# Kernel tuning notes

Measured on AMD Instinct MI355X. Metric: run time of the kernel, lower is better.

Reference implementation:

```python
import jax, jax.numpy as jnp
import numpy as np

EPS = 1e-6

def setup_inputs() -> dict:
    key = jax.random.key(0)
    ks = jax.random.split(key, 5)
    B, H, N, D = 4, 8, 8192, 64
    q = jax.random.uniform(ks[0], (B, H, N, D), dtype=jnp.float32)
    k = jax.random.uniform(ks[1], (B, H, N, D), dtype=jnp.float32)
    q_rot = jax.random.uniform(ks[2], (B, H, N, D), dtype=jnp.float32)
    k_rot = jax.random.uniform(ks[3], (B, H, N, D), dtype=jnp.float32)
    v = jax.random.normal(ks[4], (B, H, N, D), dtype=jnp.float32)
    return {"q": q, "k": k, "q_rot": q_rot, "k_rot": k_rot, "v": v, "chunk_size": 128}


def _chunked_causal_linear_attention(q, k, q_rot, k_rot, v, chunk_size):
    # Faithful port of infer_hidden_states: chunked causal linear attention
    # with cumsum kernel trick and recurrent state carry-over.
    B, H, N, D = q.shape
    E = v.shape[-1]
    C = chunk_size
    nc = N // C

    def to_chunks(x):
        # [B,H,N,d] -> [nc,B,H,C,d]
        return jnp.moveaxis(x.reshape(B, H, nc, C, x.shape[-1]), 2, 0)

    qc, kc, qrc, krc, vc = map(to_chunks, (q, k, q_rot, k_rot, v))

    init = (
        jnp.zeros((B, H, 1, D), q.dtype),        # last_k_cumsum
        jnp.zeros((B, H, 1, D, E), q.dtype),     # last_context_cumsum
        jnp.zeros((B, H, 1, D), q.dtype),        # last_k_cumsum_rot
        jnp.zeros((B, H, 1, D, E), q.dtype),     # last_context_cumsum_rot
    )

    def step(carry, inp):
        last_k, last_S, last_k_rot, last_S_rot = carry
        qi, ki, qri, kri, vi = inp                  # [B,H,C,*]
        k_cs = last_k + jnp.cumsum(ki, axis=-2)     # [B,H,C,D]
        k_cs_rot = last_k_rot + jnp.cumsum(kri, axis=-2)
        Dn = jnp.einsum('bhnd,bhnd->bhn', qi, k_cs)
        Dr = jnp.einsum('bhnd,bhnd->bhn', qri, k_cs_rot)
        D_inv = 1.0 / (Dn + Dr + EPS)               # [B,H,C]
        ctx = jnp.einsum('bhnd,bhne->bhnde', ki, vi)
        S = last_S + jnp.cumsum(ctx, axis=2)        # [B,H,C,D,E]
        ctx_rot = jnp.einsum('bhnd,bhne->bhnde', kri, vi)
        S_rot = last_S_rot + jnp.cumsum(ctx_rot, axis=2)
        out = jnp.einsum('bhnde,bhnd,bhn->bhne', S, qi, D_inv)
        out = out + jnp.einsum('bhnde,bhnd,bhn->bhne', S_rot, qri, D_inv)
        new_carry = (k_cs[:, :, -1:], S[:, :, -1:], k_cs_rot[:, :, -1:], S_rot[:, :, -1:])
        return new_carry, out

    (Z, S, Z_rot, S_rot), outs = jax.lax.scan(step, init, (qc, kc, qrc, krc, vc))
    out = jnp.moveaxis(outs, 0, 2).reshape(B, H, N, E)
    # states: squeeze chunk dim as in torch (squeeze(2))
    return out, Z[:, :, 0], S[:, :, 0], Z_rot[:, :, 0], S_rot[:, :, 0]


def reference(q, k, q_rot, k_rot, v, chunk_size):
    return _chunked_causal_linear_attention(q, k, q_rot, k_rot, v, chunk_size)
```

## Files before the change

kernel.cpp:

```cpp
#include <hip/hip_runtime.h>


typedef short bf16x8 __attribute__((ext_vector_type(8)));
typedef float f32x4  __attribute__((ext_vector_type(4)));
union U16x8 { bf16x8 v; uint4 u; };

constexpr int BH = 32;
constexpr int N_ = 8192, D_ = 64, E_ = 64, C_ = 128;
constexpr int NC = 64;
constexpr int NCHUNKS = BH * NC;
constexpr int STATE = 8320;
#define EPS_ 1e-6f

constexpr size_t OUT_ELEMS = (size_t)BH * N_ * E_;
constexpr size_t ZOFF  = OUT_ELEMS;
constexpr size_t SOFF  = ZOFF  + (size_t)BH * 64;
constexpr size_t ZROFF = SOFF  + (size_t)BH * 4096;
constexpr size_t SROFF = ZROFF + (size_t)BH * 64;

__device__ inline unsigned cvt2(float a, float b){
    union { float f; unsigned u; } x, y; x.f = a; y.f = b;
    unsigned lo = (x.u + 0x7fffu + ((x.u >> 16) & 1u)) >> 16;
    unsigned hi = (y.u + 0x7fffu + ((y.u >> 16) & 1u)) >> 16;
    return lo | (hi << 16);
}
__device__ inline unsigned short cvt1(float a){
    union { float f; unsigned u; } x; x.f = a;
    return (unsigned short)((x.u + 0x7fffu + ((x.u >> 16) & 1u)) >> 16);
}
__device__ inline float bflo(float x, unsigned short hi){
    union { unsigned u; float f; } h; h.u = ((unsigned)hi) << 16;
    return x - h.f;
}

constexpr int TILE = 520;
#define MFMA(A,B,C) __builtin_amdgcn_mfma_f32_16x16x32_bf16((A),(B),(C),0,0,0)

constexpr int AKH = 0, AKL = 8, ARH = 16, ARL = 24, BVH = 32, BVL = 40, BON = 48;
constexpr int SM1_TOT = 50 * TILE;

__global__ __launch_bounds__(256, 3) void chunk_states(
    const float* __restrict__ gk, const float* __restrict__ gkr,
    const float* __restrict__ gv, float* __restrict__ ws)
{
    __shared__ unsigned short sm[SM1_TOT];
    const int t = threadIdx.x;
    const int cid = blockIdx.x, bh = cid >> 6, c = cid & 63;
    const size_t gbase = (size_t)bh * N_ * D_ + (size_t)c * C_ * D_;
    const int w = t >> 6, lane = t & 63, lg = lane >> 4, lm = lane & 15;
    const int col = t & 63, r0g = (t >> 6) * 16;

    float kv[16], krv[16], vv[16];
    auto load_half = [&](int h){
        const size_t base = gbase + (size_t)(h * 64 + r0g) * D_ + col;
#pragma unroll
        for (int i = 0; i < 16; ++i) {
            kv [i] = gk [base + (size_t)i * D_];
            krv[i] = gkr[base + (size_t)i * D_];
            vv [i] = gv [base + (size_t)i * D_];
        }
    };
    auto write_hl = [&](const float* v16, int hiT, int loT){
#pragma unroll
        for (int hh = 0; hh < 2; ++hh) {
            const int rr = r0g + 8 * hh;
            const int tile = (rr >> 5) * 4 + (col >> 4);
            const int off = ((col & 15) + 16 * ((rr & 31) >> 3)) * 8;
            unsigned short h8[8]; float l8[8];
#pragma unroll
            for (int j = 0; j < 8; ++j) {
                h8[j] = cvt1(v16[8*hh + j]);
                l8[j] = bflo(v16[8*hh + j], h8[j]);
            }
            uint4 uh = make_uint4((unsigned)h8[0] | ((unsigned)h8[1] << 16),
                                  (unsigned)h8[2] | ((unsigned)h8[3] << 16),
                                  (unsigned)h8[4] | ((unsigned)h8[5] << 16),
                                  (unsigned)h8[6] | ((unsigned)h8[7] << 16));
            uint4 ul = make_uint4(cvt2(l8[0],l8[1]), cvt2(l8[2],l8[3]),
                                  cvt2(l8[4],l8[5]), cvt2(l8[6],l8[7]));
            *(uint4*)&sm[(hiT + tile) * TILE + off] = uh;
            *(uint4*)&sm[(loT + tile) * TILE + off] = ul;
        }
    };

    for (int i = t; i < 2 * TILE; i += 256) {
        const int tile = i / TILE, off = i % TILE;
        unsigned short val = (off < 512 && ((off >> 3) & 15) == 0) ? (unsigned short)0x3F80 : (unsigned short)0;
        sm[(BON + tile) * TILE + off] = val;
    }

    f32x4 aK[4], aR[4], sK = {0.f,0.f,0.f,0.f}, sR = {0.f,0.f,0.f,0.f};
#pragma unroll
    for (int e = 0; e < 4; ++e) { aK[e] = f32x4{0.f,0.f,0.f,0.f}; aR[e] = f32x4{0.f,0.f,0.f,0.f}; }

    auto FR = [&](int tile)->bf16x8 { return *(const bf16x8*)&sm[tile * TILE + lane * 8]; };
    auto compute = [&](){
#pragma unroll
        for (int kt = 0; kt < 2; ++kt) {
            bf16x8 ah = FR(AKH + kt*4 + w), al = FR(AKL + kt*4 + w);
            bf16x8 rh = FR(ARH + kt*4 + w), rl = FR(ARL + kt*4 + w);
            bf16x8 bo = FR(BON + kt);
            sK = MFMA(ah, bo, sK); sK = MFMA(al, bo, sK);
            sR = MFMA(rh, bo, sR); sR = MFMA(rl, bo, sR);
#pragma unroll
            for (int et = 0; et < 4; ++et) {
                bf16x8 bh = FR(BVH + kt*4 + et), bl = FR(BVL + kt*4 + et);
                aK[et] = MFMA(ah, bh, aK[et]);
                aK[et] = MFMA(al, bh, aK[et]);
                aK[et] = MFMA(ah, bl, aK[et]);
                aR[et] = MFMA(rh, bh, aR[et]);
                aR[et] = MFMA(rl, bh, aR[et]);
                aR[et] = MFMA(rh, bl, aR[et]);
            }
        }
    };

    load_half(0);
    write_hl(kv, AKH, AKL); write_hl(krv, ARH, ARL); write_hl(vv, BVH, BVL);
    load_half(1);
    __syncthreads();
    compute();
    __syncthreads();
    write_hl(kv, AKH, AKL); write_hl(krv, ARH, ARL); write_hl(vv, BVH, BVL);
    __syncthreads();
    compute();

    float* st = ws + (size_t)cid * STATE;
    if (lm == 0) {
#pragma unroll
        for (int r = 0; r < 4; ++r) {
            const int d = w*16 + lg*4 + r;
            st[d]      = sK[r];
            st[64 + d] = sR[r];
        }
    }
    float* cs  = st + 128;
    float* csr = st + 128 + 4096;
#pragma unroll
    for (int et = 0; et < 4; ++et)
#pragma unroll
        for (int r = 0; r < 4; ++r) {
            const int d = w*16 + lg*4 + r, e = et*16 + lm;
            cs [d*64 + e] = aK[et][r];
            csr[d*64 + e] = aR[et][r];
        }
}

__global__ __launch_bounds__(256) void scan_states(float* __restrict__ ws, float* __restrict__ out)
{
    const int bh = blockIdx.x;
    const int j4 = blockIdx.y * 256 + threadIdx.x;
    if (j4 >= STATE / 4) return;
    float4 run = make_float4(0.f, 0.f, 0.f, 0.f);
    float* base = ws + (size_t)bh * NC * STATE + (size_t)j4 * 4;
#pragma unroll 8
    for (int c = 0; c < NC; ++c) {
        float4 x = *(float4*)(base + (size_t)c * STATE);
        *(float4*)(base + (size_t)c * STATE) = run;
        run.x += x.x; run.y += x.y; run.z += x.z; run.w += x.w;
    }
    const int j = j4 * 4;
    float* dst;
    if (j < 64)        dst = out + ZOFF  + (size_t)bh*64   + j;
    else if (j < 128)  dst = out + ZROFF + (size_t)bh*64   + (j - 64);
    else if (j < 4224) dst = out + SOFF  + (size_t)bh*4096 + (j - 128);
    else               dst = out + SROFF + (size_t)bh*4096 + (j - 4224);
    *(float4*)dst = run;
}

constexpr int SK0 = 0, SV0 = 16, SP0 = 24, SSC0 = 0;
constexpr int SM3_TOT = 32 * TILE;

#define KFRG(ten,td,tm)  (*(const bf16x8*)&sm[(SK0 + ((ten)*2+(td))*4+(tm))*TILE + lane*8])
#define VFRG(tk,te)      (*(const bf16x8*)&sm[(SV0 + (tk)*4+(te))*TILE + lane*8])
#define SCFRG(ten,td,te) (*(const bf16x8*)&sm[(SSC0 + (ten)*10+(td)*5+(te))*TILE + lane*8])

__device__ inline void stage_colT(const float* src, int ldr, unsigned short* dst, int mr, int mc){
    const int t = threadIdx.x;
    const int col = t & 63, r0 = (t >> 6) * 16;
    float v[16];
#pragma unroll
    for (int i = 0; i < 16; ++i) v[i] = src[(size_t)(r0 + i) * ldr + col];
#pragma unroll
    for (int h = 0; h < 2; ++h) {
        const int rr = r0 + 8 * h;
        const int tile = (rr >> 5) * mr + (col >> 4) * mc;
        uint4 u = make_uint4(cvt2(v[8*h+0],v[8*h+1]), cvt2(v[8*h+2],v[8*h+3]),
                             cvt2(v[8*h+4],v[8*h+5]), cvt2(v[8*h+6],v[8*h+7]));
        *(uint4*)&dst[tile*TILE + ((col&15) + 16*((rr&31)>>3))*8] = u;
    }
}

__global__ __launch_bounds__(256, 4) void chunk_out(
    const float* __restrict__ gq, const float* __restrict__ gqr,
    const float* __restrict__ gk, const float* __restrict__ gkr,
    const float* __restrict__ gv, const float* __restrict__ ws,
    float* __restrict__ out)
{
    __shared__ unsigned short sm[SM3_TOT];
    const int t = threadIdx.x;
    const int blk = blockIdx.x, chunk = blk >> 1, rbk = blk & 1;
    const int bh = chunk >> 6, c = chunk & 63;
    const size_t gbase = (size_t)bh * N_ * D_ + (size_t)c * C_ * D_;
    const float* st = ws + (size_t)chunk * STATE;
    const int w = t >> 6, lane = t & 63, lg = lane >> 4, lm = lane & 15;
    const int col = t & 63, r0g = (t >> 6) * 16;

    bf16x8 qf[2][2];
    {
        const size_t qrow = gbase + (size_t)(rbk*64 + w*16 + lm) * D_;
#pragma unroll
        for (int td = 0; td < 2; ++td) {
            const size_t g = qrow + td*32 + lg*8;
            float4 a = *(const float4*)(gq + g),  b = *(const float4*)(gq + g + 4);
            float4 ar= *(const float4*)(gqr + g), br= *(const float4*)(gqr + g + 4);
            U16x8 u;
            u.u = make_uint4(cvt2(a.x,a.y), cvt2(a.z,a.w), cvt2(b.x,b.y), cvt2(b.z,b.w));
            qf[0][td] = u.v;
            u.u = make_uint4(cvt2(ar.x,ar.y), cvt2(ar.z,ar.w), cvt2(br.x,br.y), cvt2(br.z,br.w));
            qf[1][td] = u.v;
        }
    }

    float4 kf4[4], rf4[4];
    auto load_kr = [&](int mh){
        const size_t g = gbase + (size_t)(mh*64 + (t >> 2)) * D_ + (t & 3)*16;
#pragma unroll
        for (int i = 0; i < 4; ++i) {
            kf4[i] = *(const float4*)(gk  + g + i*4);
            rf4[i] = *(const float4*)(gkr + g + i*4);
        }
    };
    auto write_row_reg = [&](const float4* f, int baseT, int mr, int mc){
        const int r = t >> 2, c0 = (t & 3) * 16;
        const int tile = (r >> 4) * mr + (c0 >> 5) * mc;
        const int g0 = (c0 & 31) >> 3;
        uint4 u0 = make_uint4(cvt2(f[0].x,f[0].y), cvt2(f[0].z,f[0].w),
                              cvt2(f[1].x,f[1].y), cvt2(f[1].z,f[1].w));
        uint4 u1 = make_uint4(cvt2(f[2].x,f[2].y), cvt2(f[2].z,f[2].w),
                              cvt2(f[3].x,f[3].y), cvt2(f[3].z,f[3].w));
        *(uint4*)&sm[(baseT + tile)*TILE + ((r&15) + 16* g0   )*8] = u0;
        *(uint4*)&sm[(baseT + tile)*TILE + ((r&15) + 16*(g0+1))*8] = u1;
    };
    auto stage_v = [&](int mh){
        float vv[16];
        const size_t base = gbase + (size_t)(mh*64 + r0g) * D_ + col;
#pragma unroll
        for (int i = 0; i < 16; ++i) vv[i] = gv[base + (size_t)i * D_];
#pragma unroll
        for (int hh = 0; hh < 2; ++hh) {
            const int rr = r0g + 8*hh;
            const int tile = (rr >> 5) * 4 + (col >> 4);
            uint4 u = make_uint4(cvt2(vv[8*hh+0],vv[8*hh+1]), cvt2(vv[8*hh+2],vv[8*hh+3]),
                                 cvt2(vv[8*hh+4],vv[8*hh+5]), cvt2(vv[8*hh+6],vv[8*hh+7]));
            *(uint4*)&sm[(SV0 + tile)*TILE + ((col&15) + 16*((rr&31)>>3))*8] = u;
        }
    };

    f32x4 oacc[4];
#pragma unroll
    for (int te = 0; te < 4; ++te) oacc[te] = f32x4{0.f,0.f,0.f,0.f};
    f32x4 acc4 = f32x4{0.f,0.f,0.f,0.f};
    float denp[4] = {0.f,0.f,0.f,0.f};

    const int TMmax = rbk * 4 + w;
    const int TKtop = ((TMmax >> 1) << 1) + 1;

    auto compute_half = [&](int mh){
#pragma unroll
        for (int tm = 0; tm < 4; ++tm) {
            const int TM = mh*4 + tm;
            if (TM <= TKtop) {
                f32x4 a = f32x4{0.f,0.f,0.f,0.f};
                if (TM <= TMmax) {
                    a = MFMA(qf[0][0], KFRG(0,0,tm), a);
                    a = MFMA(qf[0][1], KFRG(0,1,tm), a);
                    a = MFMA(qf[1][0], KFRG(1,0,tm), a);
                    a = MFMA(qf[1][1], KFRG(1,1,tm), a);
                }
                const int mb = TM * 16 + lm;
                const int pb = (SP0 + w*2 + (tm>>1))*TILE
                             + 16*((tm&1)*2 + (lm>>3))*8 + (lm&7);
#pragma unroll
                for (int r = 0; r < 4; ++r) {
                    const int ng = rbk*64 + w*16 + lg*4 + r;
                    const float pv = (TM <= TMmax && mb <= ng) ? a[r] : 0.f;
                    denp[r] += pv;
                    sm[pb + (lg*4 + r)*8] = cvt1(pv);
                }
            }
        }
#pragma unroll
        for (int tk = 0; tk < 2; ++tk) {
            const int TK = mh*2 + tk;
            if (TK <= (TMmax >> 1)) {
                bf16x8 pa = *(const bf16x8*)&sm[(SP0 + w*2+tk)*TILE + lane*8];
#pragma unroll
                for (int te = 0; te < 4; ++te)
                    oacc[te] = MFMA(pa, VFRG(tk,te), oacc[te]);
            }
        }
    };

    load_kr(0);
    write_row_reg(kf4, SK0, 1, 4);
    write_row_reg(rf4, SK0 + 8, 1, 4);
    stage_v(0);
    if (rbk) load_kr(1);
    __syncthreads();
    compute_half(0);
    if (rbk) {
        __syncthreads();
        write_row_reg(kf4, SK0, 1, 4);
        write_row_reg(rf4, SK0 + 8, 1, 4);
        stage_v(1);
        __syncthreads();
        compute_half(1);
    }

    __syncthreads();
    stage_colT(st + 128,        64, sm + SSC0*TILE,             5, 1);
    stage_colT(st + 128 + 4096, 64, sm + (SSC0 + 10)*TILE,      5, 1);
    for (int i = t; i < 4 * 260; i += 256) {
        const int tile = i / 260, off = i % 260;
        const int ten = tile >> 1, td = tile & 1;
        *(unsigned*)&sm[(SSC0 + ten*10 + td*5 + 4)*TILE + off*2] = 0u;
    }
    __syncthreads();
    if (t < 128) {
        const int ten = t >> 6, d = t & 63;
        sm[(SSC0 + ten*10 + (d>>5)*5 + 4)*TILE + (16*((d&31)>>3))*8 + (d&7)] = cvt1(st[t]);
    }
    __syncthreads();
#pragma unroll
    for (int td = 0; td < 2; ++td) {
#pragma unroll
        for (int te = 0; te < 4; ++te) {
            oacc[te] = MFMA(qf[0][td], SCFRG(0,td,te), oacc[te]);
            oacc[te] = MFMA(qf[1][td], SCFRG(1,td,te), oacc[te]);
        }
        acc4 = MFMA(qf[0][td], SCFRG(0,td,4), acc4);
        acc4 = MFMA(qf[1][td], SCFRG(1,td,4), acc4);
    }

    const size_t orow = (size_t)bh * N_ * E_ + (size_t)(c * C_ + rbk * 64 + w * 16) * E_;
#pragma unroll
    for (int r = 0; r < 4; ++r) {
        float d = denp[r];
        d += __shfl_xor(d, 1); d += __shfl_xor(d, 2);
        d += __shfl_xor(d, 4); d += __shfl_xor(d, 8);
        const float dc = __shfl(acc4[r], lane & 48);
        const float dinv = 1.0f / (d + dc + EPS_);
        const size_t ob = orow + (size_t)(lg * 4 + r) * E_ + lm;
        out[ob +  0] = oacc[0][r] * dinv;
        out[ob + 16] = oacc[1][r] * dinv;
        out[ob + 32] = oacc[2][r] * dinv;
        out[ob + 48] = oacc[3][r] * dinv;
    }
}
#undef KFRG
#undef VFRG
#undef SCFRG

extern "C" void kernel_launch(void* const* d_in, const int* in_sizes, int n_in,
                              void* d_out, int out_size, void* d_ws, size_t ws_size,
                              hipStream_t stream) {
    const float* q  = (const float*)d_in[0];
    const float* k  = (const float*)d_in[1];
    const float* qr = (const float*)d_in[2];
    const float* kr = (const float*)d_in[3];
    const float* v  = (const float*)d_in[4];
    float* out = (float*)d_out;
    float* ws  = (float*)d_ws;

    chunk_states<<<NCHUNKS, 256, 0, stream>>>(k, kr, v, ws);
    scan_states<<<dim3(BH, 9), 256, 0, stream>>>(ws, out);
    chunk_out<<<NCHUNKS * 2, 256, 0, stream>>>(q, qr, k, kr, v, ws, out);
}
```

Measured before the change: 398.4 us.

## Merge chunk_out row halves into one 512-thread block and build constant fragments in registers

chunk_out now runs one 512-thread block per chunk instead of two 256-thread blocks that each restaged K/Kr/V. The shared K/V tiles are loaded once per half, and warps whose rows precede the current half skip its compute. The ones-fragment and the Z-augmentation fragment are now built in registers rather than staged through shared memory. Each state tile is prefetched into registers before the intra-chunk loop. This removes duplicated global loads and several syncs, at the cost of more LDS per block and load imbalance across the eight warps.

```diff
diff --git a/kernel.cpp b/kernel.cpp
--- a/kernel.cpp
+++ b/kernel.cpp
@@ -36,8 +36,8 @@
 constexpr int TILE = 520;
 #define MFMA(A,B,C) __builtin_amdgcn_mfma_f32_16x16x32_bf16((A),(B),(C),0,0,0)
 
-constexpr int AKH = 0, AKL = 8, ARH = 16, ARL = 24, BVH = 32, BVL = 40, BON = 48;
-constexpr int SM1_TOT = 50 * TILE;
+constexpr int AKH = 0, AKL = 8, ARH = 16, ARL = 24, BVH = 32, BVL = 40;
+constexpr int SM1_TOT = 48 * TILE;
 
 __global__ __launch_bounds__(256, 3) void chunk_states(
     const float* __restrict__ gk, const float* __restrict__ gkr,
@@ -49,6 +49,11 @@
     const size_t gbase = (size_t)bh * N_ * D_ + (size_t)c * C_ * D_;
     const int w = t >> 6, lane = t & 63, lg = lane >> 4, lm = lane & 15;
     const int col = t & 63, r0g = (t >> 6) * 16;
+
+    U16x8 uo;
+    uo.u = (lm == 0) ? make_uint4(0x3F803F80u,0x3F803F80u,0x3F803F80u,0x3F803F80u)
+                     : make_uint4(0u,0u,0u,0u);
+    const bf16x8 onesf = uo.v;
 
     float kv[16], krv[16], vv[16];
     auto load_half = [&](int h){
@@ -83,12 +88,6 @@
         }
     };
 
-    for (int i = t; i < 2 * TILE; i += 256) {
-        const int tile = i / TILE, off = i % TILE;
-        unsigned short val = (off < 512 && ((off >> 3) & 15) == 0) ? (unsigned short)0x3F80 : (unsigned short)0;
-        sm[(BON + tile) * TILE + off] = val;
-    }
-
     f32x4 aK[4], aR[4], sK = {0.f,0.f,0.f,0.f}, sR = {0.f,0.f,0.f,0.f};
 #pragma unroll
     for (int e = 0; e < 4; ++e) { aK[e] = f32x4{0.f,0.f,0.f,0.f}; aR[e] = f32x4{0.f,0.f,0.f,0.f}; }
@@ -99,9 +98,8 @@
         for (int kt = 0; kt < 2; ++kt) {
             bf16x8 ah = FR(AKH + kt*4 + w), al = FR(AKL + kt*4 + w);
             bf16x8 rh = FR(ARH + kt*4 + w), rl = FR(ARL + kt*4 + w);
-            bf16x8 bo = FR(BON + kt);
-            sK = MFMA(ah, bo, sK); sK = MFMA(al, bo, sK);
-            sR = MFMA(rh, bo, sR); sR = MFMA(rl, bo, sR);
+            sK = MFMA(ah, onesf, sK); sK = MFMA(al, onesf, sK);
+            sR = MFMA(rh, onesf, sR); sR = MFMA(rl, onesf, sR);
 #pragma unroll
             for (int et = 0; et < 4; ++et) {
                 bf16x8 bh = FR(BVH + kt*4 + et), bl = FR(BVL + kt*4 + et);
@@ -168,30 +166,14 @@
     *(float4*)dst = run;
 }
 
-constexpr int SK0 = 0, SV0 = 16, SP0 = 24, SSC0 = 0;
-constexpr int SM3_TOT = 32 * TILE;
+constexpr int SK0 = 0, SV0 = 16, SP0 = 24;
+constexpr int SM3_TOT = 40 * TILE;
 
 #define KFRG(ten,td,tm)  (*(const bf16x8*)&sm[(SK0 + ((ten)*2+(td))*4+(tm))*TILE + lane*8])
 #define VFRG(tk,te)      (*(const bf16x8*)&sm[(SV0 + (tk)*4+(te))*TILE + lane*8])
-#define SCFRG(ten,td,te) (*(const bf16x8*)&sm[(SSC0 + (ten)*10+(td)*5+(te))*TILE + lane*8])
-
-__device__ inline void stage_colT(const float* src, int ldr, unsigned short* dst, int mr, int mc){
-    const int t = threadIdx.x;
-    const int col = t & 63, r0 = (t >> 6) * 16;
-    float v[16];
-#pragma unroll
-    for (int i = 0; i < 16; ++i) v[i] = src[(size_t)(r0 + i) * ldr + col];
-#pragma unroll
-    for (int h = 0; h < 2; ++h) {
-        const int rr = r0 + 8 * h;
-        const int tile = (rr >> 5) * mr + (col >> 4) * mc;
-        uint4 u = make_uint4(cvt2(v[8*h+0],v[8*h+1]), cvt2(v[8*h+2],v[8*h+3]),
-                             cvt2(v[8*h+4],v[8*h+5]), cvt2(v[8*h+6],v[8*h+7]));
-        *(uint4*)&dst[tile*TILE + ((col&15) + 16*((rr&31)>>3))*8] = u;
-    }
-}
-
-__global__ __launch_bounds__(256, 4) void chunk_out(
+#define SCFRG(ten,td,te) (*(const bf16x8*)&sm[((ten)*8+(td)*4+(te))*TILE + lane*8])
+
+__global__ __launch_bounds__(512, 6) void chunk_out(
     const float* __restrict__ gq, const float* __restrict__ gqr,
     const float* __restrict__ gk, const float* __restrict__ gkr,
     const float* __restrict__ gv, const float* __restrict__ ws,
@@ -199,16 +181,15 @@
 {
     __shared__ unsigned short sm[SM3_TOT];
     const int t = threadIdx.x;
-    const int blk = blockIdx.x, chunk = blk >> 1, rbk = blk & 1;
+    const int chunk = blockIdx.x;
     const int bh = chunk >> 6, c = chunk & 63;
     const size_t gbase = (size_t)bh * N_ * D_ + (size_t)c * C_ * D_;
     const float* st = ws + (size_t)chunk * STATE;
     const int w = t >> 6, lane = t & 63, lg = lane >> 4, lm = lane & 15;
-    const int col = t & 63, r0g = (t >> 6) * 16;
 
     bf16x8 qf[2][2];
     {
-        const size_t qrow = gbase + (size_t)(rbk*64 + w*16 + lm) * D_;
+        const size_t qrow = gbase + (size_t)(w*16 + lm) * D_;
 #pragma unroll
         for (int td = 0; td < 2; ++td) {
             const size_t g = qrow + td*32 + lg*8;
@@ -222,40 +203,14 @@
         }
     }
 
-    float4 kf4[4], rf4[4];
-    auto load_kr = [&](int mh){
-        const size_t g = gbase + (size_t)(mh*64 + (t >> 2)) * D_ + (t & 3)*16;
-#pragma unroll
-        for (int i = 0; i < 4; ++i) {
-            kf4[i] = *(const float4*)(gk  + g + i*4);
-            rf4[i] = *(const float4*)(gkr + g + i*4);
-        }
-    };
-    auto write_row_reg = [&](const float4* f, int baseT, int mr, int mc){
-        const int r = t >> 2, c0 = (t & 3) * 16;
-        const int tile = (r >> 4) * mr + (c0 >> 5) * mc;
-        const int g0 = (c0 & 31) >> 3;
-        uint4 u0 = make_uint4(cvt2(f[0].x,f[0].y), cvt2(f[0].z,f[0].w),
-                              cvt2(f[1].x,f[1].y), cvt2(f[1].z,f[1].w));
-        uint4 u1 = make_uint4(cvt2(f[2].x,f[2].y), cvt2(f[2].z,f[2].w),
-                              cvt2(f[3].x,f[3].y), cvt2(f[3].z,f[3].w));
-        *(uint4*)&sm[(baseT + tile)*TILE + ((r&15) + 16* g0   )*8] = u0;
-        *(uint4*)&sm[(baseT + tile)*TILE + ((r&15) + 16*(g0+1))*8] = u1;
-    };
-    auto stage_v = [&](int mh){
-        float vv[16];
-        const size_t base = gbase + (size_t)(mh*64 + r0g) * D_ + col;
-#pragma unroll
-        for (int i = 0; i < 16; ++i) vv[i] = gv[base + (size_t)i * D_];
-#pragma unroll
-        for (int hh = 0; hh < 2; ++hh) {
-            const int rr = r0g + 8*hh;
-            const int tile = (rr >> 5) * 4 + (col >> 4);
-            uint4 u = make_uint4(cvt2(vv[8*hh+0],vv[8*hh+1]), cvt2(vv[8*hh+2],vv[8*hh+3]),
-                                 cvt2(vv[8*hh+4],vv[8*hh+5]), cvt2(vv[8*hh+6],vv[8*hh+7]));
-            *(uint4*)&sm[(SV0 + tile)*TILE + ((col&15) + 16*((rr&31)>>3))*8] = u;
-        }
-    };
+    float sc8[8], scr8[8];
+    {
+        const int col = t & 63, r0 = (t >> 6) * 8;
+        const float* p  = st + 128        + (size_t)r0 * 64 + col;
+        const float* pr = st + 128 + 4096 + (size_t)r0 * 64 + col;
+#pragma unroll
+        for (int i = 0; i < 8; ++i) { sc8[i] = p[i*64]; scr8[i] = pr[i*64]; }
+    }
 
     f32x4 oacc[4];
 #pragma unroll
@@ -263,75 +218,96 @@
     f32x4 acc4 = f32x4{0.f,0.f,0.f,0.f};
     float denp[4] = {0.f,0.f,0.f,0.f};
 
-    const int TMmax = rbk * 4 + w;
-    const int TKtop = ((TMmax >> 1) << 1) + 1;
-
-    auto compute_half = [&](int mh){
-#pragma unroll
-        for (int tm = 0; tm < 4; ++tm) {
-            const int TM = mh*4 + tm;
-            if (TM <= TKtop) {
-                f32x4 a = f32x4{0.f,0.f,0.f,0.f};
-                if (TM <= TMmax) {
-                    a = MFMA(qf[0][0], KFRG(0,0,tm), a);
-                    a = MFMA(qf[0][1], KFRG(0,1,tm), a);
-                    a = MFMA(qf[1][0], KFRG(1,0,tm), a);
-                    a = MFMA(qf[1][1], KFRG(1,1,tm), a);
-                }
-                const int mb = TM * 16 + lm;
-                const int pb = (SP0 + w*2 + (tm>>1))*TILE
-                             + 16*((tm&1)*2 + (lm>>3))*8 + (lm&7);
-#pragma unroll
-                for (int r = 0; r < 4; ++r) {
-                    const int ng = rbk*64 + w*16 + lg*4 + r;
-                    const float pv = (TM <= TMmax && mb <= ng) ? a[r] : 0.f;
-                    denp[r] += pv;
-                    sm[pb + (lg*4 + r)*8] = cvt1(pv);
+    const int TKtop = ((w >> 1) << 1) + 1;
+
+    for (int mh = 0; mh < 2; ++mh) {
+        __syncthreads();
+        {
+            const int r = t >> 3, c0 = (t & 7) * 8;
+            const size_t g = gbase + (size_t)(mh*64 + r) * D_ + c0;
+            const int tb  = (r >> 4) + (c0 >> 5) * 4;
+            const int off = ((r & 15) + 16 * ((c0 & 31) >> 3)) * 8;
+            float4 a = *(const float4*)(gk + g), b = *(const float4*)(gk + g + 4);
+            *(uint4*)&sm[(SK0 + tb)*TILE + off] =
+                make_uint4(cvt2(a.x,a.y), cvt2(a.z,a.w), cvt2(b.x,b.y), cvt2(b.z,b.w));
+            a = *(const float4*)(gkr + g); b = *(const float4*)(gkr + g + 4);
+            *(uint4*)&sm[(SK0 + 8 + tb)*TILE + off] =
+                make_uint4(cvt2(a.x,a.y), cvt2(a.z,a.w), cvt2(b.x,b.y), cvt2(b.z,b.w));
+        }
+        {
+            const int col = t & 63, r0 = (t >> 6) * 8;
+            const size_t vb = gbase + (size_t)(mh*64 + r0) * D_ + col;
+            float vv[8];
+#pragma unroll
+            for (int i = 0; i < 8; ++i) vv[i] = gv[vb + (size_t)i * D_];
+            const int tb  = (r0 >> 5) * 4 + (col >> 4);
+            const int off = ((col & 15) + 16 * ((r0 & 31) >> 3)) * 8;
+            *(uint4*)&sm[(SV0 + tb)*TILE + off] =
+                make_uint4(cvt2(vv[0],vv[1]), cvt2(vv[2],vv[3]),
+                           cvt2(vv[4],vv[5]), cvt2(vv[6],vv[7]));
+        }
+        __syncthreads();
+        if (w >= mh * 4) {
+#pragma unroll
+            for (int tm = 0; tm < 4; ++tm) {
+                const int TM = mh*4 + tm;
+                if (TM <= TKtop) {
+                    f32x4 a = f32x4{0.f,0.f,0.f,0.f};
+                    if (TM <= w) {
+                        a = MFMA(qf[0][0], KFRG(0,0,tm), a);
+                        a = MFMA(qf[0][1], KFRG(0,1,tm), a);
+                        a = MFMA(qf[1][0], KFRG(1,0,tm), a);
+                        a = MFMA(qf[1][1], KFRG(1,1,tm), a);
+                    }
+                    const int mb = TM * 16 + lm;
+                    const int pb = (SP0 + w*2 + (tm>>1))*TILE
+                                 + 16*((tm&1)*2 + (lm>>3))*8 + (lm&7);
+#pragma unroll
+                    for (int r = 0; r < 4; ++r) {
+                        const int ng = w*16 + lg*4 + r;
+                        const float pv = (TM <= w && mb <= ng) ? a[r] : 0.f;
+                        denp[r] += pv;
+                        sm[pb + (lg*4 + r)*8] = cvt1(pv);
+                    }
                 }
             }
-        }
-#pragma unroll
-        for (int tk = 0; tk < 2; ++tk) {
-            const int TK = mh*2 + tk;
-            if (TK <= (TMmax >> 1)) {
-                bf16x8 pa = *(const bf16x8*)&sm[(SP0 + w*2+tk)*TILE + lane*8];
-#pragma unroll
-                for (int te = 0; te < 4; ++te)
-                    oacc[te] = MFMA(pa, VFRG(tk,te), oacc[te]);
+#pragma unroll
+            for (int tk = 0; tk < 2; ++tk) {
+                if (mh*2 + tk <= (w >> 1)) {
+                    bf16x8 pa = *(const bf16x8*)&sm[(SP0 + w*2 + tk)*TILE + lane*8];
+#pragma unroll
+                    for (int te = 0; te < 4; ++te)
+                        oacc[te] = MFMA(pa, VFRG(tk,te), oacc[te]);
+                }
             }
         }
-    };
-
-    load_kr(0);
-    write_row_reg(kf4, SK0, 1, 4);
-    write_row_reg(rf4, SK0 + 8, 1, 4);
-    stage_v(0);
-    if (rbk) load_kr(1);
-    __syncthreads();
-    compute_half(0);
-    if (rbk) {
-        __syncthreads();
-        write_row_reg(kf4, SK0, 1, 4);
-        write_row_reg(rf4, SK0 + 8, 1, 4);
-        stage_v(1);
-        __syncthreads();
-        compute_half(1);
-    }
-
-    __syncthreads();
-    stage_colT(st + 128,        64, sm + SSC0*TILE,             5, 1);
-    stage_colT(st + 128 + 4096, 64, sm + (SSC0 + 10)*TILE,      5, 1);
-    for (int i = t; i < 4 * 260; i += 256) {
-        const int tile = i / 260, off = i % 260;
-        const int ten = tile >> 1, td = tile & 1;
-        *(unsigned*)&sm[(SSC0 + ten*10 + td*5 + 4)*TILE + off*2] = 0u;
-    }
-    __syncthreads();
-    if (t < 128) {
-        const int ten = t >> 6, d = t & 63;
-        sm[(SSC0 + ten*10 + (d>>5)*5 + 4)*TILE + (16*((d&31)>>3))*8 + (d&7)] = cvt1(st[t]);
-    }
-    __syncthreads();
+    }
+
+    __syncthreads();
+    {
+        const int col = t & 63, r0 = (t >> 6) * 8;
+        const int tb  = (r0 >> 5) * 4 + (col >> 4);
+        const int off = ((col & 15) + 16 * ((r0 & 31) >> 3)) * 8;
+        *(uint4*)&sm[tb*TILE + off] =
+            make_uint4(cvt2(sc8[0],sc8[1]), cvt2(sc8[2],sc8[3]),
+                       cvt2(sc8[4],sc8[5]), cvt2(sc8[6],sc8[7]));
+        *(uint4*)&sm[(8 + tb)*TILE + off] =
+            make_uint4(cvt2(scr8[0],scr8[1]), cvt2(scr8[2],scr8[3]),
+                       cvt2(scr8[4],scr8[5]), cvt2(scr8[6],scr8[7]));
+    }
+    __syncthreads();
+    bf16x8 augf[2][2];
+#pragma unroll
+    for (int ten = 0; ten < 2; ++ten)
+#pragma unroll
+        for (int td = 0; td < 2; ++td) {
+            const float* ap = st + ten*64 + td*32 + lg*8;
+            float4 a = *(const float4*)ap, b = *(const float4*)(ap + 4);
+            U16x8 u;
+            u.u = make_uint4(cvt2(a.x,a.y), cvt2(a.z,a.w), cvt2(b.x,b.y), cvt2(b.z,b.w));
+            if (lm != 0) u.u = make_uint4(0u,0u,0u,0u);
+            augf[ten][td] = u.v;
+        }
 #pragma unroll
     for (int td = 0; td < 2; ++td) {
 #pragma unroll
@@ -339,11 +315,11 @@
             oacc[te] = MFMA(qf[0][td], SCFRG(0,td,te), oacc[te]);
             oacc[te] = MFMA(qf[1][td], SCFRG(1,td,te), oacc[te]);
         }
-        acc4 = MFMA(qf[0][td], SCFRG(0,td,4), acc4);
-        acc4 = MFMA(qf[1][td], SCFRG(1,td,4), acc4);
-    }
-
-    const size_t orow = (size_t)bh * N_ * E_ + (size_t)(c * C_ + rbk * 64 + w * 16) * E_;
+        acc4 = MFMA(qf[0][td], augf[0][td], acc4);
+        acc4 = MFMA(qf[1][td], augf[1][td], acc4);
+    }
+
+    const size_t orow = (size_t)bh * N_ * E_ + (size_t)(c * C_ + w * 16) * E_;
 #pragma unroll
     for (int r = 0; r < 4; ++r) {
         float d = denp[r];
@@ -375,5 +351,5 @@
 
     chunk_states<<<NCHUNKS, 256, 0, stream>>>(k, kr, v, ws);
     scan_states<<<dim3(BH, 9), 256, 0, stream>>>(ws, out);
-    chunk_out<<<NCHUNKS * 2, 256, 0, stream>>>(q, qr, k, kr, v, ws, out);
-}
+    chunk_out<<<NCHUNKS, 512, 0, stream>>>(q, qr, k, kr, v, ws, out);
+}
```

Measured after the change: 392.4 us. About the same (-1.5%).
